# Optimization experiments

Measured on AMD Instinct MI355X. Metric: run time of the kernel, lower is better.

## Reference

```python
import jax, jax.numpy as jnp
import numpy as np

B, C, H, W = 4, 64, 160, 160
OUT = 64
KS = (5, 7)


def conv2d(x, w, b=None, pad=0, groups=1):
    y = jax.lax.conv_general_dilated(
        x, w, (1, 1), [(pad, pad), (pad, pad)],
        feature_group_count=groups,
        dimension_numbers=('NCHW', 'OIHW', 'NCHW'))
    return y if b is None else y + b[None, :, None, None]


def bn_eval(x, g, b, m, v, eps=1e-5):
    s = g / jnp.sqrt(v + eps)
    return x * s[None, :, None, None] + (b - m * s)[None, :, None, None]


def boundary_attn(x, w1, b1, w2, b2):
    Cc = x.shape[1]
    kx = jnp.array([[-1., 0., 1.], [-2., 0., 2.], [-1., 0., 1.]], jnp.float32)
    ky = jnp.array([[-1., -2., -1.], [0., 0., 0.], [1., 2., 1.]], jnp.float32)
    sobel = jnp.concatenate([jnp.tile(kx[None, None], (Cc, 1, 1, 1)),
                             jnp.tile(ky[None, None], (Cc, 1, 1, 1))], axis=0)  # [2C,1,3,3]
    # grouped conv (groups=C): same output-channel grouping semantics as torch
    edge = jnp.abs(conv2d(x, sobel, pad=1, groups=Cc))
    edge = (edge[:, :Cc] + edge[:, Cc:]).mean(axis=1, keepdims=True)
    a = jax.nn.relu(conv2d(x, w1, b1, pad=1))
    a = conv2d(a, w2, b2, pad=0)
    a = jax.nn.sigmoid(a + edge)
    return x * a + x


def icc(off, half_k):
    # iterative cumulative constraint over the (small, static) K channel axis
    K = off.shape[1]
    cs = [None] * K
    cs[half_k] = off[:, half_k]
    for i in range(1, half_k + 1):
        cs[half_k - i] = 0.5 * cs[half_k - i + 1] + 0.5 * off[:, half_k - i]
        cs[half_k + i] = 0.5 * cs[half_k + i - 1] + 0.5 * off[:, half_k + i]
    c = jnp.stack(cs, axis=1)
    w = jnp.ones((K, 1, 3, 3), jnp.float32) / 9.0
    return conv2d(c, w, pad=1, groups=K)


def tumor_center(x):
    _, _, Hx, Wx = x.shape
    fs = x.mean(axis=1)  # [B,H,W]
    hg = jnp.arange(Hx, dtype=x.dtype)[None, :, None]
    wg = jnp.arange(Wx, dtype=x.dtype)[None, None, :]
    tot = fs.sum(axis=(1, 2)) + 1e-6
    return (fs * hg).sum(axis=(1, 2)) / tot, (fs * wg).sum(axis=(1, 2)) / tot


def dyn1d(x, kw, kb, K, O):
    # Original Dynamic1DConv reshapes x to [B*H*W, C, 1, 1] and grid_samples a
    # [1,K] grid per pixel. With align_corners=True a 1x1 input maps every grid
    # coordinate to ix=iy=0, so sampled[n,c,k] == x[b,c,h,w] for all k; the
    # bmm with per-pixel kernels followed by sum over C therefore collapses to
    # (sum_c x) * (sum_k kernels) -- same math, no giant gather materialized.
    Bx, _, Hx, Wx = x.shape
    ker = conv2d(x, kw, kb, pad=0).reshape(Bx, O, K, Hx, Wx)
    return x.sum(axis=1, keepdims=True) * ker.sum(axis=2)


def reference(x, ba_w1, ba_b1, ba_w2, ba_b2,
              off_w1, off_b1, off_bn_g, off_bn_b, off_bn_m, off_bn_v,
              off_w2, off_b2,
              rk5_w, rk5_b, rk7_w, rk7_b,
              lk5_w, lk5_b, lk7_w, lk7_b,
              sf_w, sf_b, sf_bn_g, sf_bn_b, sf_bn_m, sf_bn_v,
              fc_w, fc_b):
    residual = x  # in_channels == out_channels -> nn.Identity
    xa = boundary_attn(x, ba_w1, ba_b1, ba_w2, ba_b2)
    # offset branch (faithful to original; mathematically dead because the
    # per-pixel grid_sample ignores its grid -- see dyn1d). BN in eval mode.
    raw = conv2d(xa, off_w1, off_b1, pad=1)
    raw = jax.nn.relu(bn_eval(raw, off_bn_g, off_bn_b, off_bn_m, off_bn_v))
    raw = conv2d(raw, off_w2, off_b2, pad=1)
    sumk, idx = sum(KS), 0
    _offs = []
    for k in KS:
        _offs.append(icc(jnp.tanh(raw[:, idx:idx + k]), k // 2))
        _offs.append(icc(jnp.tanh(raw[:, sumk + idx:sumk + idx + k]), k // 2))
        idx += k
    _hc, _wc = tumor_center(xa)  # also dead w.r.t. output
    O = OUT // 2 // len(KS)  # 16 channels per scale per flow type
    feats = [dyn1d(xa, rk5_w, rk5_b, 5, O), dyn1d(xa, rk7_w, rk7_b, 7, O),
             dyn1d(xa, lk5_w, lk5_b, 5, O), dyn1d(xa, lk7_w, lk7_b, 7, O)]
    fusion = jnp.concatenate(feats, axis=1)  # [B, OUT, H, W]
    y = jax.nn.relu(bn_eval(conv2d(fusion, sf_w, sf_b, pad=1),
                            sf_bn_g, sf_bn_b, sf_bn_m, sf_bn_v))
    y = conv2d(y, fc_w, fc_b, pad=0)
    return y + residual


def setup_inputs() -> dict:
    key = jax.random.key(0)
    keys = iter(jax.random.split(key, 40))
    def nrm(shape, s=0.05):
        return jax.random.normal(next(keys), shape, jnp.float32) * s
    d = {}
    d['x'] = nrm((B, C, H, W), 1.0)
    d['ba_w1'] = nrm((C // 2, C, 3, 3)); d['ba_b1'] = nrm((C // 2,))
    d['ba_w2'] = nrm((1, C // 2, 1, 1)); d['ba_b2'] = nrm((1,))
    d['off_w1'] = nrm((C // 2, C, 3, 3)); d['off_b1'] = nrm((C // 2,))
    d['off_bn_g'] = 1.0 + nrm((C // 2,)); d['off_bn_b'] = nrm((C // 2,))
    d['off_bn_m'] = nrm((C // 2,))
    d['off_bn_v'] = jax.random.uniform(next(keys), (C // 2,), jnp.float32, 0.5, 1.5)
    d['off_w2'] = nrm((2 * sum(KS), C // 2, 3, 3)); d['off_b2'] = nrm((2 * sum(KS),))
    O = OUT // 2 // len(KS)
    for name, k in (('rk5', 5), ('rk7', 7), ('lk5', 5), ('lk7', 7)):
        d[name + '_w'] = nrm((O * k, C, 1, 1)); d[name + '_b'] = nrm((O * k,))
    d['sf_w'] = nrm((OUT, OUT, 3, 3)); d['sf_b'] = nrm((OUT,))
    d['sf_bn_g'] = 1.0 + nrm((OUT,)); d['sf_bn_b'] = nrm((OUT,))
    d['sf_bn_m'] = nrm((OUT,))
    d['sf_bn_v'] = jax.random.uniform(next(keys), (OUT,), jnp.float32, 0.5, 1.5)
    d['fc_w'] = nrm((OUT, OUT, 1, 1)); d['fc_b'] = nrm((OUT,))
    return d
```

## Files before the change

kernel.cpp:

```cpp
#include <hip/hip_runtime.h>
#include <hip/hip_bf16.h>
#include <math.h>

#define BB 4
#define CC 64
#define HH 160
#define WW 160
#define HWs (HH*WW)
#define NPIX (BB*HWs)

using bf16 = __hip_bfloat16;
typedef __attribute__((ext_vector_type(8))) short short8v;
typedef __attribute__((ext_vector_type(4))) float float4v;

__device__ __forceinline__ unsigned short f2bfu(float f){
    union { bf16 h; unsigned short u; } cv; cv.h = __float2bfloat16(f); return cv.u;
}
__device__ __forceinline__ float bfu2f(unsigned short u){
    union { float f; unsigned int i; } cv; cv.i = ((unsigned int)u)<<16; return cv.f;
}

constexpr int B1X1 = 0;
constexpr int SFBo = 64;
constexpr int SFWf = 128;
constexpr int BAWf = 18560;
constexpr int FUWf = 27776;
constexpr int FCWf = 29824;
constexpr int WS_FLOATS = 31872;

__global__ void k_prep(const float* __restrict__ rk5w, const float* __restrict__ rk5b,
                       const float* __restrict__ rk7w, const float* __restrict__ rk7b,
                       const float* __restrict__ lk5w, const float* __restrict__ lk5b,
                       const float* __restrict__ lk7w, const float* __restrict__ lk7b,
                       const float* __restrict__ sfw,  const float* __restrict__ sfb,
                       const float* __restrict__ bng,  const float* __restrict__ bnb,
                       const float* __restrict__ bnm,  const float* __restrict__ bnv,
                       const float* __restrict__ baw1, const float* __restrict__ fcw,
                       float* __restrict__ ws)
{
    int tid = blockIdx.x*blockDim.x + threadIdx.x;
    int nt  = gridDim.x*blockDim.x;
    for(int o=tid;o<64;o+=nt){
        int grp=o>>4, oo=o&15; int K=(grp&1)?7:5;
        const float* bp = (grp==0)?rk5b:(grp==1)?rk7b:(grp==2)?lk5b:lk7b;
        float s=0.f; for(int k=0;k<K;k++) s += bp[oo*K+k];
        ws[B1X1+o]=s;
    }
    for(int oc=tid;oc<64;oc+=nt){
        float sc = bng[oc]*rsqrtf(bnv[oc]+1e-5f);
        ws[SFBo+oc] = sfb[oc]*sc + bnb[oc] - bnm[oc]*sc;
    }
    unsigned short* sfwf = (unsigned short*)(ws + SFWf);
    for(int idx=tid; idx<36864; idx+=nt){
        int og = idx/9216;  int rem = idx - og*9216;
        int tp = rem/1024;  int rem2 = rem - tp*1024;
        int kc = rem2>>9;   int rem3 = rem2 & 511;
        int lane = rem3>>3; int j = rem3&7;
        int oc = og*16 + (lane&15);
        int ic = kc*32 + (lane>>4)*8 + j;
        float sc = bng[oc]*rsqrtf(bnv[oc]+1e-5f);
        sfwf[idx] = f2bfu(sfw[(oc*64+ic)*9 + tp] * sc);
    }
    unsigned short* bawf = (unsigned short*)(ws + BAWf);
    for(int idx=tid; idx<18432; idx+=nt){
        int og = idx/9216;  int r1 = idx - og*9216;
        int f  = r1/512;    int r2 = r1 & 511;
        int lane = r2>>3;   int j = r2&7;
        int tap = f>>1, kc = f&1;
        int oc = og*16 + (lane&15);
        int ic = kc*32 + (lane>>4)*8 + j;
        bawf[idx] = f2bfu(baw1[(oc*64+ic)*9 + tap]);
    }
    unsigned short* fuwf = (unsigned short*)(ws + FUWf);
    for(int idx=tid; idx<4096; idx+=nt){
        int wave = idx>>10;
        int kc   = (idx>>9)&1;
        int lane = (idx>>3)&63;
        int j    = idx&7;
        int oc = wave*16 + (lane&15);
        int c  = kc*32 + (lane>>4)*8 + j;
        int oo = oc&15; int K = (wave&1)?7:5;
        const float* w = (wave==0)?rk5w:(wave==1)?rk7w:(wave==2)?lk5w:lk7w;
        float s = 0.f;
        for(int k=0;k<K;k++) s += w[(oo*K+k)*64 + c];
        fuwf[idx] = f2bfu(s);
    }
    unsigned short* fcwf = (unsigned short*)(ws + FCWf);
    for(int idx=tid; idx<4096; idx+=nt){
        int wave = idx>>10;
        int kc   = (idx>>9)&1;
        int lane = (idx>>3)&63;
        int j    = idx&7;
        int oc = wave*16 + (lane&15);
        int c  = kc*32 + (lane>>4)*8 + j;
        fcwf[idx] = f2bfu(fcw[oc*64 + c]);
    }
}

__global__ __launch_bounds__(256)
void k_x2nhwc(const float* __restrict__ x, unsigned short* __restrict__ xb)
{
    __shared__ unsigned short ls[128*72];
    const int t = threadIdx.x;
    const int p0 = blockIdx.x*128;
    const int b = p0 / HWs, pp0 = p0 % HWs;
    const float* xbase = x + (size_t)b*CC*HWs + pp0;
    #pragma unroll
    for(int iter=0; iter<32; iter++){
        int idx = iter*256 + t;
        int c = idx>>7, px = idx&127;
        int bs = (c>>3) ^ ((px>>3)&7);
        ls[px*72 + bs*8 + (c&7)] = f2bfu(xbase[(size_t)c*HWs + px]);
    }
    __syncthreads();
    #pragma unroll
    for(int iter=0; iter<4; iter++){
        int idx = iter*256 + t;
        int sub = idx&7, px = idx>>3;
        int bs = sub ^ ((px>>3)&7);
        short8v v = *(short8v*)(ls + px*72 + bs*8);
        *(short8v*)(xb + ((size_t)(p0+px))*64 + sub*8) = v;
    }
}

__global__ __launch_bounds__(256)
void k_fuseA(const unsigned short* __restrict__ xb, const float* __restrict__ bab1,
             const float* __restrict__ baw2, const float* __restrict__ bab2,
             const float* __restrict__ ws, unsigned short* __restrict__ fus)
{
    __shared__ unsigned short tile[10*18*72];
    __shared__ float zbuf[2][8][16];
    __shared__ float ebuf[2][128];
    __shared__ float sxbuf[8][16];
    __shared__ float pbuf[128], qbuf[128];
    const int bw = blockIdx.x, bh = blockIdx.y, b = blockIdx.z;
    const int t = threadIdx.x;
    const int wave = t>>6, lane = t&63;
    const int quad = lane>>4, n = lane&15;
    const int og = wave&1, rh = wave>>1;
    const int w0 = bw*16, h0 = bh*8;

    const unsigned short* fb = xb + (size_t)b*HWs*64;
    for(int idx=t; idx<1440; idx+=256){
        int sub = idx&7; int pix = idx>>3;
        int row = pix/18, col = pix%18;
        int gh = h0-1+row, gw = w0-1+col;
        short8v v = {0,0,0,0,0,0,0,0};
        if(gh>=0&&gh<HH&&gw>=0&&gw<WW)
            v = *(const short8v*)(fb + ((size_t)(gh*WW+gw))*64 + sub*8);
        *(short8v*)(tile + (row*18+col)*72 + sub*8) = v;
    }
    const unsigned short* bawf = (const unsigned short*)(ws + BAWf);
    short8v afrag[18];
    #pragma unroll
    for(int f=0; f<18; f++)
        afrag[f] = *(const short8v*)(bawf + (((size_t)og*18 + f)*64 + lane)*8);
    const unsigned short* fuwf = (const unsigned short*)(ws + FUWf);
    short8v wfrag[2];
    #pragma unroll
    for(int kc=0; kc<2; kc++)
        wfrag[kc] = *(const short8v*)(fuwf + (((size_t)wave*2 + kc)*64 + lane)*8);
    short8v ones;
    #pragma unroll
    for(int j=0;j<8;j++) ones[j] = (short)0x3F80;
    float b1[4], w2[4], bq[4];
    #pragma unroll
    for(int r=0;r<4;r++){
        b1[r] = bab1[og*16 + quad*4 + r];
        w2[r] = baw2[og*16 + quad*4 + r];
        bq[r] = ws[B1X1 + wave*16 + quad*4 + r];
    }
    __syncthreads();

    #pragma unroll
    for(int srp=0; srp<2; srp++){
        const int gr0 = rh*4 + srp*2, gr1 = gr0+1;
        float4v acc0={0,0,0,0}, acc1={0,0,0,0};
        #pragma unroll
        for(int tap=0; tap<9; tap++){
            const int dh = tap/3, dw = tap%3;
            const unsigned short* base0 = tile + ((gr0+dh)*18 + dw + n)*72 + quad*8;
            const unsigned short* base1 = tile + ((gr1+dh)*18 + dw + n)*72 + quad*8;
            #pragma unroll
            for(int kc=0; kc<2; kc++){
                short8v v0 = *(const short8v*)(base0 + kc*32);
                short8v v1 = *(const short8v*)(base1 + kc*32);
                acc0 = __builtin_amdgcn_mfma_f32_16x16x32_bf16(afrag[tap*2+kc], v0, acc0, 0,0,0);
                acc1 = __builtin_amdgcn_mfma_f32_16x16x32_bf16(afrag[tap*2+kc], v1, acc1, 0,0,0);
            }
        }
        float c0 = 0.f, c1 = 0.f;
        #pragma unroll
        for(int r=0;r<4;r++){
            c0 += fmaxf(acc0[r] + b1[r], 0.f) * w2[r];
            c1 += fmaxf(acc1[r] + b1[r], 0.f) * w2[r];
        }
        c0 += __shfl_xor(c0, 16); c0 += __shfl_xor(c0, 32);
        c1 += __shfl_xor(c1, 16); c1 += __shfl_xor(c1, 32);
        if(lane < 16){
            zbuf[og][gr0][lane] = c0;
            zbuf[og][gr1][lane] = c1;
        }
    }

    {
        const int r0 = wave*2, r1 = wave*2+1;
        float4v sa0={0,0,0,0}, sa1={0,0,0,0};
        #pragma unroll
        for(int kc=0; kc<2; kc++){
            short8v v0 = *(const short8v*)(tile + ((r0+1)*18 + 1 + n)*72 + quad*8 + kc*32);
            short8v v1 = *(const short8v*)(tile + ((r1+1)*18 + 1 + n)*72 + quad*8 + kc*32);
            sa0 = __builtin_amdgcn_mfma_f32_16x16x32_bf16(ones, v0, sa0, 0,0,0);
            sa1 = __builtin_amdgcn_mfma_f32_16x16x32_bf16(ones, v1, sa1, 0,0,0);
        }
        if(lane < 16){
            sxbuf[r0][lane] = sa0[0];
            sxbuf[r1][lane] = sa1[0];
        }
    }

    {
        const int half = t>>7, px = t&127;
        const int r = px>>4, c = px&15;
        float e = 0.f;
        #pragma unroll
        for(int s=0; s<4; s++){
            const int sub = half*4 + s;
            if(half==0){
                short8v a0 = *(const short8v*)(tile + ((r  )*18 + c  )*72 + sub*8);
                short8v a2 = *(const short8v*)(tile + ((r  )*18 + c+2)*72 + sub*8);
                short8v a3 = *(const short8v*)(tile + ((r+1)*18 + c  )*72 + sub*8);
                short8v a5 = *(const short8v*)(tile + ((r+1)*18 + c+2)*72 + sub*8);
                short8v a6 = *(const short8v*)(tile + ((r+2)*18 + c  )*72 + sub*8);
                short8v a8 = *(const short8v*)(tile + ((r+2)*18 + c+2)*72 + sub*8);
                #pragma unroll
                for(int j=0;j<8;j++){
                    float gx = (bfu2f((unsigned short)a2[j]) - bfu2f((unsigned short)a0[j]))
                       + 2.f*(bfu2f((unsigned short)a5[j]) - bfu2f((unsigned short)a3[j]))
                       +      (bfu2f((unsigned short)a8[j]) - bfu2f((unsigned short)a6[j]));
                    e += fabsf(gx);
                }
            } else {
                short8v b0 = *(const short8v*)(tile + ((r  )*18 + c  )*72 + sub*8);
                short8v b1v= *(const short8v*)(tile + ((r  )*18 + c+1)*72 + sub*8);
                short8v b2 = *(const short8v*)(tile + ((r  )*18 + c+2)*72 + sub*8);
                short8v b6 = *(const short8v*)(tile + ((r+2)*18 + c  )*72 + sub*8);
                short8v b7 = *(const short8v*)(tile + ((r+2)*18 + c+1)*72 + sub*8);
                short8v b8 = *(const short8v*)(tile + ((r+2)*18 + c+2)*72 + sub*8);
                #pragma unroll
                for(int j=0;j<8;j++){
                    float gy = (bfu2f((unsigned short)b6[j]) - bfu2f((unsigned short)b0[j]))
                       + 2.f*(bfu2f((unsigned short)b7[j]) - bfu2f((unsigned short)b1v[j]))
                       +      (bfu2f((unsigned short)b8[j]) - bfu2f((unsigned short)b2[j]));
                    e += fabsf(gy);
                }
            }
        }
        ebuf[half][px] = e;
    }
    __syncthreads();

    if(t < 128){
        const int row = t>>4, col = t&15;
        float z = zbuf[0][row][col] + zbuf[1][row][col] + bab2[0]
                + (ebuf[0][t] + ebuf[1][t]) * (1.f/32.f);
        float A = 1.f + 1.f/(1.f+__expf(-z));
        float S = A * sxbuf[row][col];
        pbuf[t] = A*S;
        qbuf[t] = S;
    }
    __syncthreads();

    #pragma unroll
    for(int srp=0; srp<4; srp++){
        const int r0 = srp*2, r1 = srp*2+1;
        float4v acc0={0,0,0,0}, acc1={0,0,0,0};
        #pragma unroll
        for(int kc=0; kc<2; kc++){
            short8v v0 = *(const short8v*)(tile + ((r0+1)*18 + 1 + n)*72 + quad*8 + kc*32);
            short8v v1 = *(const short8v*)(tile + ((r1+1)*18 + 1 + n)*72 + quad*8 + kc*32);
            acc0 = __builtin_amdgcn_mfma_f32_16x16x32_bf16(wfrag[kc], v0, acc0, 0,0,0);
            acc1 = __builtin_amdgcn_mfma_f32_16x16x32_bf16(wfrag[kc], v1, acc1, 0,0,0);
        }
        union { unsigned long long u; unsigned short s[4]; } pk0, pk1;
        const int px0 = r0*16 + n, px1 = r1*16 + n;
        const float P0 = pbuf[px0], Q0 = qbuf[px0];
        const float P1 = pbuf[px1], Q1 = qbuf[px1];
        #pragma unroll
        for(int r=0;r<4;r++){
            pk0.s[r] = f2bfu(P0*acc0[r] + Q0*bq[r]);
            pk1.s[r] = f2bfu(P1*acc1[r] + Q1*bq[r]);
        }
        unsigned short* fp0 = fus + ((size_t)b*HWs + (h0+r0)*WW + w0 + n)*64 + wave*16 + quad*4;
        unsigned short* fp1 = fus + ((size_t)b*HWs + (h0+r1)*WW + w0 + n)*64 + wave*16 + quad*4;
        *(unsigned long long*)fp0 = pk0.u;
        *(unsigned long long*)fp1 = pk1.u;
    }
}

__global__ __launch_bounds__(256)
void k_fuseB(const unsigned short* __restrict__ fus, const float* __restrict__ ws,
             const float* __restrict__ fcb, const float* __restrict__ x,
             float* __restrict__ out)
{
    __shared__ unsigned short ftile[10*18*72];
    __shared__ unsigned short ytile[128*72];
    const int bw = blockIdx.x, bh = blockIdx.y, b = blockIdx.z;
    const int t  = threadIdx.x;
    const int wave = t>>6, lane = t&63;
    const int quad = lane>>4, n = lane&15;
    const int w0 = bw*16, h0 = bh*8;

    const unsigned short* fb = fus + (size_t)b*HWs*64;
    for(int idx=t; idx<1440; idx+=256){
        int sub = idx&7; int pix = idx>>3;
        int row = pix/18, col = pix%18;
        int gh = h0-1+row, gw = w0-1+col;
        short8v v = {0,0,0,0,0,0,0,0};
        if(gh>=0&&gh<HH&&gw>=0&&gw<WW)
            v = *(const short8v*)(fb + ((size_t)(gh*WW+gw))*64 + sub*8);
        *(short8v*)(ftile + (row*18+col)*72 + sub*8) = v;
    }
    const unsigned short* sfwf = (const unsigned short*)(ws + SFWf);
    short8v afrag[18];
    #pragma unroll
    for(int f=0; f<18; f++)
        afrag[f] = *(const short8v*)(sfwf + (((size_t)wave*18 + f)*64 + lane)*8);
    const unsigned short* fcwf = (const unsigned short*)(ws + FCWf);
    short8v ffrag[2];
    #pragma unroll
    for(int kc=0; kc<2; kc++)
        ffrag[kc] = *(const short8v*)(fcwf + (((size_t)wave*2 + kc)*64 + lane)*8);
    float bias[4], fb4[4];
    #pragma unroll
    for(int r=0;r<4;r++){
        bias[r] = ws[SFBo + wave*16 + quad*4 + r];
        fb4[r]  = fcb[wave*16 + quad*4 + r];
    }
    __syncthreads();

    #pragma unroll
    for(int srp=0; srp<4; srp++){
        const int r0 = srp*2, r1 = srp*2+1;
        float4v acc0={0,0,0,0}, acc1={0,0,0,0};
        #pragma unroll
        for(int tap=0; tap<9; tap++){
            const int dh = tap/3, dw = tap%3;
            const unsigned short* base0 = ftile + ((r0+dh)*18 + dw + n)*72 + quad*8;
            const unsigned short* base1 = ftile + ((r1+dh)*18 + dw + n)*72 + quad*8;
            #pragma unroll
            for(int kc=0; kc<2; kc++){
                short8v b0 = *(const short8v*)(base0 + kc*32);
                short8v b1 = *(const short8v*)(base1 + kc*32);
                acc0 = __builtin_amdgcn_mfma_f32_16x16x32_bf16(afrag[tap*2+kc], b0, acc0, 0,0,0);
                acc1 = __builtin_amdgcn_mfma_f32_16x16x32_bf16(afrag[tap*2+kc], b1, acc1, 0,0,0);
            }
        }
        union { unsigned long long u; unsigned short s[4]; } pk0, pk1;
        #pragma unroll
        for(int r=0;r<4;r++){
            pk0.s[r] = f2bfu(fmaxf(acc0[r] + bias[r], 0.f));
            pk1.s[r] = f2bfu(fmaxf(acc1[r] + bias[r], 0.f));
        }
        *(unsigned long long*)(ytile + (r0*16+n)*72 + wave*16 + quad*4) = pk0.u;
        *(unsigned long long*)(ytile + (r1*16+n)*72 + wave*16 + quad*4) = pk1.u;
    }
    __syncthreads();

    #pragma unroll
    for(int srp=0; srp<4; srp++){
        const int r0 = srp*2, r1 = srp*2+1;
        float4v acc0={0,0,0,0}, acc1={0,0,0,0};
        #pragma unroll
        for(int kc=0; kc<2; kc++){
            short8v b0 = *(const short8v*)(ytile + (r0*16+n)*72 + quad*8 + kc*32);
            short8v b1 = *(const short8v*)(ytile + (r1*16+n)*72 + quad*8 + kc*32);
            acc0 = __builtin_amdgcn_mfma_f32_16x16x32_bf16(ffrag[kc], b0, acc0, 0,0,0);
            acc1 = __builtin_amdgcn_mfma_f32_16x16x32_bf16(ffrag[kc], b1, acc1, 0,0,0);
        }
        #pragma unroll
        for(int r=0;r<4;r++){
            int oc = wave*16 + quad*4 + r;
            size_t g0 = ((size_t)(b*CC + oc))*HWs + (h0+r0)*WW + w0 + n;
            size_t g1 = ((size_t)(b*CC + oc))*HWs + (h0+r1)*WW + w0 + n;
            out[g0] = acc0[r] + fb4[r] + x[g0];
            out[g1] = acc1[r] + fb4[r] + x[g1];
        }
    }
}

extern "C" void kernel_launch(void* const* d_in, const int* in_sizes, int n_in,
                              void* d_out, int out_size, void* d_ws, size_t ws_size,
                              hipStream_t stream)
{
    const float* x     = (const float*)d_in[0];
    const float* ba_w1 = (const float*)d_in[1];
    const float* ba_b1 = (const float*)d_in[2];
    const float* ba_w2 = (const float*)d_in[3];
    const float* ba_b2 = (const float*)d_in[4];
    const float* rk5_w = (const float*)d_in[13];
    const float* rk5_b = (const float*)d_in[14];
    const float* rk7_w = (const float*)d_in[15];
    const float* rk7_b = (const float*)d_in[16];
    const float* lk5_w = (const float*)d_in[17];
    const float* lk5_b = (const float*)d_in[18];
    const float* lk7_w = (const float*)d_in[19];
    const float* lk7_b = (const float*)d_in[20];
    const float* sf_w  = (const float*)d_in[21];
    const float* sf_b  = (const float*)d_in[22];
    const float* bng   = (const float*)d_in[23];
    const float* bnb   = (const float*)d_in[24];
    const float* bnm   = (const float*)d_in[25];
    const float* bnv   = (const float*)d_in[26];
    const float* fc_w  = (const float*)d_in[27];
    const float* fc_b  = (const float*)d_in[28];

    float* wsf = (float*)d_ws;
    unsigned short* XB  = (unsigned short*)((char*)d_ws + (size_t)WS_FLOATS*4);
    unsigned short* FUS = XB + (size_t)NPIX*64;
    float* out = (float*)d_out;

    k_prep<<<64, 256, 0, stream>>>(rk5_w,rk5_b,rk7_w,rk7_b,lk5_w,lk5_b,lk7_w,lk7_b,
                                   sf_w,sf_b,bng,bnb,bnm,bnv, ba_w1, fc_w, wsf);
    k_x2nhwc<<<NPIX/128, 256, 0, stream>>>(x, XB);
    k_fuseA<<<dim3(10,20,4), 256, 0, stream>>>(XB, ba_b1, ba_w2, ba_b2, wsf, FUS);
    k_fuseB<<<dim3(10,20,4), 256, 0, stream>>>(FUS, wsf, fc_b, x, out);
}
```

Baseline: 182.2 us.

## Switch fused conv kernels from 16x16x32 to 32x32x16 bf16 MFMA tiles

Reorganizes the weight-fragment layouts and the MFMA loops in the boundary-attention, fusion and spatial-fuse kernels to use 32x32x16 bf16 MFMA instructions in place of 16x16x32. Each wave now covers 32 output channels by 32 pixels (two rows of sixteen), and the two-output-group zbuf reduction collapses to one. The aim is to cut the number of MFMA issues and LDS B-fragment reads per output. In exchange it needs larger float16 accumulators, repacks weights per k-chunk, and loads the A fragments per k-chunk inside the loop instead of once up front.

```diff
diff --git a/kernel.cpp b/kernel.cpp
--- a/kernel.cpp
+++ b/kernel.cpp
@@ -10,14 +10,20 @@
 #define NPIX (BB*HWs)
 
 using bf16 = __hip_bfloat16;
-typedef __attribute__((ext_vector_type(8))) short short8v;
-typedef __attribute__((ext_vector_type(4))) float float4v;
+typedef __attribute__((ext_vector_type(8)))  short short8v;
+typedef __attribute__((ext_vector_type(16))) float float16v;
 
 __device__ __forceinline__ unsigned short f2bfu(float f){
     union { bf16 h; unsigned short u; } cv; cv.h = __float2bfloat16(f); return cv.u;
 }
 __device__ __forceinline__ float bfu2f(unsigned short u){
     union { float f; unsigned int i; } cv; cv.i = ((unsigned int)u)<<16; return cv.f;
+}
+__device__ __forceinline__ float16v fzero16(){
+    float16v z;
+    #pragma unroll
+    for(int i=0;i<16;i++) z[i]=0.f;
+    return z;
 }
 
 constexpr int B1X1 = 0;
@@ -52,47 +58,46 @@
     }
     unsigned short* sfwf = (unsigned short*)(ws + SFWf);
     for(int idx=tid; idx<36864; idx+=nt){
-        int og = idx/9216;  int rem = idx - og*9216;
-        int tp = rem/1024;  int rem2 = rem - tp*1024;
-        int kc = rem2>>9;   int rem3 = rem2 & 511;
-        int lane = rem3>>3; int j = rem3&7;
-        int oc = og*16 + (lane&15);
-        int ic = kc*32 + (lane>>4)*8 + j;
+        int og = idx/18432;  int rem = idx - og*18432;
+        int f  = rem>>9;     int r2 = rem & 511;
+        int lane = r2>>3;    int j = r2&7;
+        int tap = f>>2, kc = f&3;
+        int oc = og*32 + (lane&31);
+        int ic = kc*16 + (lane>>5)*8 + j;
         float sc = bng[oc]*rsqrtf(bnv[oc]+1e-5f);
-        sfwf[idx] = f2bfu(sfw[(oc*64+ic)*9 + tp] * sc);
+        sfwf[idx] = f2bfu(sfw[(oc*64+ic)*9 + tap] * sc);
     }
     unsigned short* bawf = (unsigned short*)(ws + BAWf);
     for(int idx=tid; idx<18432; idx+=nt){
-        int og = idx/9216;  int r1 = idx - og*9216;
-        int f  = r1/512;    int r2 = r1 & 511;
-        int lane = r2>>3;   int j = r2&7;
-        int tap = f>>1, kc = f&1;
-        int oc = og*16 + (lane&15);
-        int ic = kc*32 + (lane>>4)*8 + j;
+        int f  = idx>>9;     int r2 = idx & 511;
+        int lane = r2>>3;    int j = r2&7;
+        int tap = f>>2, kc = f&3;
+        int oc = lane&31;
+        int ic = kc*16 + (lane>>5)*8 + j;
         bawf[idx] = f2bfu(baw1[(oc*64+ic)*9 + tap]);
     }
     unsigned short* fuwf = (unsigned short*)(ws + FUWf);
     for(int idx=tid; idx<4096; idx+=nt){
-        int wave = idx>>10;
-        int kc   = (idx>>9)&1;
+        int og   = idx>>11;
+        int kc   = (idx>>9)&3;
         int lane = (idx>>3)&63;
         int j    = idx&7;
-        int oc = wave*16 + (lane&15);
-        int c  = kc*32 + (lane>>4)*8 + j;
-        int oo = oc&15; int K = (wave&1)?7:5;
-        const float* w = (wave==0)?rk5w:(wave==1)?rk7w:(wave==2)?lk5w:lk7w;
+        int oc = og*32 + (lane&31);
+        int c  = kc*16 + (lane>>5)*8 + j;
+        int grp = oc>>4, oo = oc&15; int K = (grp&1)?7:5;
+        const float* w = (grp==0)?rk5w:(grp==1)?rk7w:(grp==2)?lk5w:lk7w;
         float s = 0.f;
         for(int k=0;k<K;k++) s += w[(oo*K+k)*64 + c];
         fuwf[idx] = f2bfu(s);
     }
     unsigned short* fcwf = (unsigned short*)(ws + FCWf);
     for(int idx=tid; idx<4096; idx+=nt){
-        int wave = idx>>10;
-        int kc   = (idx>>9)&1;
+        int og   = idx>>11;
+        int kc   = (idx>>9)&3;
         int lane = (idx>>3)&63;
         int j    = idx&7;
-        int oc = wave*16 + (lane&15);
-        int c  = kc*32 + (lane>>4)*8 + j;
+        int oc = og*32 + (lane&31);
+        int c  = kc*16 + (lane>>5)*8 + j;
         fcwf[idx] = f2bfu(fcw[oc*64 + c]);
     }
 }
@@ -129,15 +134,14 @@
              const float* __restrict__ ws, unsigned short* __restrict__ fus)
 {
     __shared__ unsigned short tile[10*18*72];
-    __shared__ float zbuf[2][8][16];
+    __shared__ float zbuf[8][16];
     __shared__ float ebuf[2][128];
     __shared__ float sxbuf[8][16];
     __shared__ float pbuf[128], qbuf[128];
     const int bw = blockIdx.x, bh = blockIdx.y, b = blockIdx.z;
     const int t = threadIdx.x;
     const int wave = t>>6, lane = t&63;
-    const int quad = lane>>4, n = lane&15;
-    const int og = wave&1, rh = wave>>1;
+    const int half = lane>>5, n = lane&31;
     const int w0 = bw*16, h0 = bh*8;
 
     const unsigned short* fb = xb + (size_t)b*HWs*64;
@@ -150,83 +154,61 @@
             v = *(const short8v*)(fb + ((size_t)(gh*WW+gw))*64 + sub*8);
         *(short8v*)(tile + (row*18+col)*72 + sub*8) = v;
     }
+    float b1v[16], w2v[16];
+    #pragma unroll
+    for(int r=0;r<16;r++){
+        int oc = (r&3) + 8*(r>>2) + 4*half;
+        b1v[r] = bab1[oc];
+        w2v[r] = baw2[oc];
+    }
+    __syncthreads();
+
     const unsigned short* bawf = (const unsigned short*)(ws + BAWf);
-    short8v afrag[18];
-    #pragma unroll
-    for(int f=0; f<18; f++)
-        afrag[f] = *(const short8v*)(bawf + (((size_t)og*18 + f)*64 + lane)*8);
-    const unsigned short* fuwf = (const unsigned short*)(ws + FUWf);
-    short8v wfrag[2];
-    #pragma unroll
-    for(int kc=0; kc<2; kc++)
-        wfrag[kc] = *(const short8v*)(fuwf + (((size_t)wave*2 + kc)*64 + lane)*8);
-    short8v ones;
-    #pragma unroll
-    for(int j=0;j<8;j++) ones[j] = (short)0x3F80;
-    float b1[4], w2[4], bq[4];
-    #pragma unroll
-    for(int r=0;r<4;r++){
-        b1[r] = bab1[og*16 + quad*4 + r];
-        w2[r] = baw2[og*16 + quad*4 + r];
-        bq[r] = ws[B1X1 + wave*16 + quad*4 + r];
-    }
-    __syncthreads();
-
-    #pragma unroll
-    for(int srp=0; srp<2; srp++){
-        const int gr0 = rh*4 + srp*2, gr1 = gr0+1;
-        float4v acc0={0,0,0,0}, acc1={0,0,0,0};
-        #pragma unroll
-        for(int tap=0; tap<9; tap++){
-            const int dh = tap/3, dw = tap%3;
-            const unsigned short* base0 = tile + ((gr0+dh)*18 + dw + n)*72 + quad*8;
-            const unsigned short* base1 = tile + ((gr1+dh)*18 + dw + n)*72 + quad*8;
-            #pragma unroll
-            for(int kc=0; kc<2; kc++){
-                short8v v0 = *(const short8v*)(base0 + kc*32);
-                short8v v1 = *(const short8v*)(base1 + kc*32);
-                acc0 = __builtin_amdgcn_mfma_f32_16x16x32_bf16(afrag[tap*2+kc], v0, acc0, 0,0,0);
-                acc1 = __builtin_amdgcn_mfma_f32_16x16x32_bf16(afrag[tap*2+kc], v1, acc1, 0,0,0);
-            }
-        }
-        float c0 = 0.f, c1 = 0.f;
-        #pragma unroll
-        for(int r=0;r<4;r++){
-            c0 += fmaxf(acc0[r] + b1[r], 0.f) * w2[r];
-            c1 += fmaxf(acc1[r] + b1[r], 0.f) * w2[r];
-        }
-        c0 += __shfl_xor(c0, 16); c0 += __shfl_xor(c0, 32);
-        c1 += __shfl_xor(c1, 16); c1 += __shfl_xor(c1, 32);
-        if(lane < 16){
-            zbuf[og][gr0][lane] = c0;
-            zbuf[og][gr1][lane] = c1;
-        }
-    }
-
-    {
-        const int r0 = wave*2, r1 = wave*2+1;
-        float4v sa0={0,0,0,0}, sa1={0,0,0,0};
-        #pragma unroll
-        for(int kc=0; kc<2; kc++){
-            short8v v0 = *(const short8v*)(tile + ((r0+1)*18 + 1 + n)*72 + quad*8 + kc*32);
-            short8v v1 = *(const short8v*)(tile + ((r1+1)*18 + 1 + n)*72 + quad*8 + kc*32);
-            sa0 = __builtin_amdgcn_mfma_f32_16x16x32_bf16(ones, v0, sa0, 0,0,0);
-            sa1 = __builtin_amdgcn_mfma_f32_16x16x32_bf16(ones, v1, sa1, 0,0,0);
-        }
-        if(lane < 16){
-            sxbuf[r0][lane] = sa0[0];
-            sxbuf[r1][lane] = sa1[0];
-        }
-    }
-
-    {
-        const int half = t>>7, px = t&127;
+    {
+        const int rbase = 2*wave + (n>>4);
+        const int cbase = n&15;
+        float16v acc = fzero16();
+        #pragma unroll
+        for(int kc=0; kc<4; kc++){
+            short8v af[9];
+            #pragma unroll
+            for(int tap=0; tap<9; tap++)
+                af[tap] = *(const short8v*)(bawf + (((size_t)(tap*4+kc))*64 + lane)*8);
+            #pragma unroll
+            for(int tap=0; tap<9; tap++){
+                const int dh = tap/3, dw = tap%3;
+                short8v bf = *(const short8v*)(tile + ((rbase+dh)*18 + cbase+dw)*72
+                                               + kc*16 + half*8);
+                acc = __builtin_amdgcn_mfma_f32_32x32x16_bf16(af[tap], bf, acc, 0,0,0);
+            }
+        }
+        float cz = 0.f;
+        #pragma unroll
+        for(int r=0;r<16;r++) cz += fmaxf(acc[r]+b1v[r],0.f)*w2v[r];
+        cz += __shfl_xor(cz, 32);
+        if(lane < 32) zbuf[2*wave + (n>>4)][n&15] = cz;
+    }
+    {
+        short8v ones;
+        #pragma unroll
+        for(int j=0;j<8;j++) ones[j] = (short)0x3F80;
+        float16v s = fzero16();
+        const int rr = 2*wave + (n>>4) + 1, cc = (n&15) + 1;
+        #pragma unroll
+        for(int kc=0; kc<4; kc++){
+            short8v bf = *(const short8v*)(tile + (rr*18 + cc)*72 + kc*16 + half*8);
+            s = __builtin_amdgcn_mfma_f32_32x32x16_bf16(ones, bf, s, 0,0,0);
+        }
+        if(lane < 32) sxbuf[2*wave + (n>>4)][n&15] = s[0];
+    }
+    {
+        const int hf = t>>7, px = t&127;
         const int r = px>>4, c = px&15;
         float e = 0.f;
         #pragma unroll
         for(int s=0; s<4; s++){
-            const int sub = half*4 + s;
-            if(half==0){
+            const int sub = hf*4 + s;
+            if(hf==0){
                 short8v a0 = *(const short8v*)(tile + ((r  )*18 + c  )*72 + sub*8);
                 short8v a2 = *(const short8v*)(tile + ((r  )*18 + c+2)*72 + sub*8);
                 short8v a3 = *(const short8v*)(tile + ((r+1)*18 + c  )*72 + sub*8);
@@ -242,7 +224,7 @@
                 }
             } else {
                 short8v b0 = *(const short8v*)(tile + ((r  )*18 + c  )*72 + sub*8);
-                short8v b1v= *(const short8v*)(tile + ((r  )*18 + c+1)*72 + sub*8);
+                short8v b1 = *(const short8v*)(tile + ((r  )*18 + c+1)*72 + sub*8);
                 short8v b2 = *(const short8v*)(tile + ((r  )*18 + c+2)*72 + sub*8);
                 short8v b6 = *(const short8v*)(tile + ((r+2)*18 + c  )*72 + sub*8);
                 short8v b7 = *(const short8v*)(tile + ((r+2)*18 + c+1)*72 + sub*8);
@@ -250,19 +232,19 @@
                 #pragma unroll
                 for(int j=0;j<8;j++){
                     float gy = (bfu2f((unsigned short)b6[j]) - bfu2f((unsigned short)b0[j]))
-                       + 2.f*(bfu2f((unsigned short)b7[j]) - bfu2f((unsigned short)b1v[j]))
+                       + 2.f*(bfu2f((unsigned short)b7[j]) - bfu2f((unsigned short)b1[j]))
                        +      (bfu2f((unsigned short)b8[j]) - bfu2f((unsigned short)b2[j]));
                     e += fabsf(gy);
                 }
             }
         }
-        ebuf[half][px] = e;
+        ebuf[hf][px] = e;
     }
     __syncthreads();
 
     if(t < 128){
         const int row = t>>4, col = t&15;
-        float z = zbuf[0][row][col] + zbuf[1][row][col] + bab2[0]
+        float z = zbuf[row][col] + bab2[0]
                 + (ebuf[0][t] + ebuf[1][t]) * (1.f/32.f);
         float A = 1.f + 1.f/(1.f+__expf(-z));
         float S = A * sxbuf[row][col];
@@ -271,30 +253,39 @@
     }
     __syncthreads();
 
-    #pragma unroll
-    for(int srp=0; srp<4; srp++){
-        const int r0 = srp*2, r1 = srp*2+1;
-        float4v acc0={0,0,0,0}, acc1={0,0,0,0};
-        #pragma unroll
-        for(int kc=0; kc<2; kc++){
-            short8v v0 = *(const short8v*)(tile + ((r0+1)*18 + 1 + n)*72 + quad*8 + kc*32);
-            short8v v1 = *(const short8v*)(tile + ((r1+1)*18 + 1 + n)*72 + quad*8 + kc*32);
-            acc0 = __builtin_amdgcn_mfma_f32_16x16x32_bf16(wfrag[kc], v0, acc0, 0,0,0);
-            acc1 = __builtin_amdgcn_mfma_f32_16x16x32_bf16(wfrag[kc], v1, acc1, 0,0,0);
-        }
-        union { unsigned long long u; unsigned short s[4]; } pk0, pk1;
-        const int px0 = r0*16 + n, px1 = r1*16 + n;
-        const float P0 = pbuf[px0], Q0 = qbuf[px0];
-        const float P1 = pbuf[px1], Q1 = qbuf[px1];
-        #pragma unroll
-        for(int r=0;r<4;r++){
-            pk0.s[r] = f2bfu(P0*acc0[r] + Q0*bq[r]);
-            pk1.s[r] = f2bfu(P1*acc1[r] + Q1*bq[r]);
-        }
-        unsigned short* fp0 = fus + ((size_t)b*HWs + (h0+r0)*WW + w0 + n)*64 + wave*16 + quad*4;
-        unsigned short* fp1 = fus + ((size_t)b*HWs + (h0+r1)*WW + w0 + n)*64 + wave*16 + quad*4;
-        *(unsigned long long*)fp0 = pk0.u;
-        *(unsigned long long*)fp1 = pk1.u;
+    {
+        const int og = wave&1;
+        const unsigned short* fuwf = (const unsigned short*)(ws + FUWf);
+        short8v wf[4];
+        #pragma unroll
+        for(int kc=0; kc<4; kc++)
+            wf[kc] = *(const short8v*)(fuwf + (((size_t)og*4 + kc)*64 + lane)*8);
+        float bqv[16];
+        #pragma unroll
+        for(int r=0;r<16;r++) bqv[r] = ws[B1X1 + og*32 + (r&3)+8*(r>>2)+4*half];
+        #pragma unroll
+        for(int t2=0; t2<2; t2++){
+            const int rp = (wave>>1) + 2*t2;
+            const int row = 2*rp + (n>>4), col = n&15;
+            float16v a = fzero16();
+            #pragma unroll
+            for(int kc=0; kc<4; kc++){
+                short8v bf = *(const short8v*)(tile + ((row+1)*18 + col+1)*72
+                                               + kc*16 + half*8);
+                a = __builtin_amdgcn_mfma_f32_32x32x16_bf16(wf[kc], bf, a, 0,0,0);
+            }
+            const float P = pbuf[row*16+col], Q = qbuf[row*16+col];
+            unsigned short* base = fus + ((size_t)b*HWs + (h0+row)*WW + w0+col)*64
+                                   + og*32 + 4*half;
+            #pragma unroll
+            for(int g=0; g<4; g++){
+                union { unsigned long long u; unsigned short s[4]; } pk;
+                #pragma unroll
+                for(int rr=0; rr<4; rr++)
+                    pk.s[rr] = f2bfu(P*a[4*g+rr] + Q*bqv[4*g+rr]);
+                *(unsigned long long*)(base + 8*g) = pk.u;
+            }
+        }
     }
 }
 
@@ -308,7 +299,8 @@
     const int bw = blockIdx.x, bh = blockIdx.y, b = blockIdx.z;
     const int t  = threadIdx.x;
     const int wave = t>>6, lane = t&63;
-    const int quad = lane>>4, n = lane&15;
+    const int half = lane>>5, n = lane&31;
+    const int og = wave&1;
     const int w0 = bw*16, h0 = bh*8;
 
     const unsigned short* fb = fus + (size_t)b*HWs*64;
@@ -321,70 +313,75 @@
             v = *(const short8v*)(fb + ((size_t)(gh*WW+gw))*64 + sub*8);
         *(short8v*)(ftile + (row*18+col)*72 + sub*8) = v;
     }
+    float biasv[16];
+    #pragma unroll
+    for(int r=0;r<16;r++) biasv[r] = ws[SFBo + og*32 + (r&3)+8*(r>>2)+4*half];
+    __syncthreads();
+
     const unsigned short* sfwf = (const unsigned short*)(ws + SFWf);
-    short8v afrag[18];
-    #pragma unroll
-    for(int f=0; f<18; f++)
-        afrag[f] = *(const short8v*)(sfwf + (((size_t)wave*18 + f)*64 + lane)*8);
-    const unsigned short* fcwf = (const unsigned short*)(ws + FCWf);
-    short8v ffrag[2];
-    #pragma unroll
-    for(int kc=0; kc<2; kc++)
-        ffrag[kc] = *(const short8v*)(fcwf + (((size_t)wave*2 + kc)*64 + lane)*8);
-    float bias[4], fb4[4];
-    #pragma unroll
-    for(int r=0;r<4;r++){
-        bias[r] = ws[SFBo + wave*16 + quad*4 + r];
-        fb4[r]  = fcb[wave*16 + quad*4 + r];
-    }
-    __syncthreads();
-
-    #pragma unroll
-    for(int srp=0; srp<4; srp++){
-        const int r0 = srp*2, r1 = srp*2+1;
-        float4v acc0={0,0,0,0}, acc1={0,0,0,0};
-        #pragma unroll
-        for(int tap=0; tap<9; tap++){
-            const int dh = tap/3, dw = tap%3;
-            const unsigned short* base0 = ftile + ((r0+dh)*18 + dw + n)*72 + quad*8;
-            const unsigned short* base1 = ftile + ((r1+dh)*18 + dw + n)*72 + quad*8;
-            #pragma unroll
-            for(int kc=0; kc<2; kc++){
-                short8v b0 = *(const short8v*)(base0 + kc*32);
-                short8v b1 = *(const short8v*)(base1 + kc*32);
-                acc0 = __builtin_amdgcn_mfma_f32_16x16x32_bf16(afrag[tap*2+kc], b0, acc0, 0,0,0);
-                acc1 = __builtin_amdgcn_mfma_f32_16x16x32_bf16(afrag[tap*2+kc], b1, acc1, 0,0,0);
-            }
-        }
-        union { unsigned long long u; unsigned short s[4]; } pk0, pk1;
-        #pragma unroll
-        for(int r=0;r<4;r++){
-            pk0.s[r] = f2bfu(fmaxf(acc0[r] + bias[r], 0.f));
-            pk1.s[r] = f2bfu(fmaxf(acc1[r] + bias[r], 0.f));
-        }
-        *(unsigned long long*)(ytile + (r0*16+n)*72 + wave*16 + quad*4) = pk0.u;
-        *(unsigned long long*)(ytile + (r1*16+n)*72 + wave*16 + quad*4) = pk1.u;
-    }
-    __syncthreads();
-
-    #pragma unroll
-    for(int srp=0; srp<4; srp++){
-        const int r0 = srp*2, r1 = srp*2+1;
-        float4v acc0={0,0,0,0}, acc1={0,0,0,0};
-        #pragma unroll
-        for(int kc=0; kc<2; kc++){
-            short8v b0 = *(const short8v*)(ytile + (r0*16+n)*72 + quad*8 + kc*32);
-            short8v b1 = *(const short8v*)(ytile + (r1*16+n)*72 + quad*8 + kc*32);
-            acc0 = __builtin_amdgcn_mfma_f32_16x16x32_bf16(ffrag[kc], b0, acc0, 0,0,0);
-            acc1 = __builtin_amdgcn_mfma_f32_16x16x32_bf16(ffrag[kc], b1, acc1, 0,0,0);
-        }
-        #pragma unroll
-        for(int r=0;r<4;r++){
-            int oc = wave*16 + quad*4 + r;
-            size_t g0 = ((size_t)(b*CC + oc))*HWs + (h0+r0)*WW + w0 + n;
-            size_t g1 = ((size_t)(b*CC + oc))*HWs + (h0+r1)*WW + w0 + n;
-            out[g0] = acc0[r] + fb4[r] + x[g0];
-            out[g1] = acc1[r] + fb4[r] + x[g1];
+    const int rp0 = wave>>1, rp1 = rp0+2;
+    const int row0 = 2*rp0 + (n>>4), row1 = 2*rp1 + (n>>4), col = n&15;
+    {
+        float16v A0 = fzero16(), A1 = fzero16();
+        #pragma unroll
+        for(int kc=0; kc<4; kc++){
+            short8v af[9];
+            #pragma unroll
+            for(int tap=0; tap<9; tap++)
+                af[tap] = *(const short8v*)(sfwf + (((size_t)og*36 + tap*4+kc)*64 + lane)*8);
+            #pragma unroll
+            for(int tap=0; tap<9; tap++){
+                const int dh = tap/3, dw = tap%3;
+                short8v b0 = *(const short8v*)(ftile + ((row0+dh)*18 + col+dw)*72
+                                               + kc*16 + half*8);
+                short8v b1 = *(const short8v*)(ftile + ((row1+dh)*18 + col+dw)*72
+                                               + kc*16 + half*8);
+                A0 = __builtin_amdgcn_mfma_f32_32x32x16_bf16(af[tap], b0, A0, 0,0,0);
+                A1 = __builtin_amdgcn_mfma_f32_32x32x16_bf16(af[tap], b1, A1, 0,0,0);
+            }
+        }
+        unsigned short* y0 = ytile + (row0*16+col)*72 + og*32 + 4*half;
+        unsigned short* y1p = ytile + (row1*16+col)*72 + og*32 + 4*half;
+        #pragma unroll
+        for(int g=0; g<4; g++){
+            union { unsigned long long u; unsigned short s[4]; } pk0, pk1;
+            #pragma unroll
+            for(int rr=0; rr<4; rr++){
+                pk0.s[rr] = f2bfu(fmaxf(A0[4*g+rr] + biasv[4*g+rr], 0.f));
+                pk1.s[rr] = f2bfu(fmaxf(A1[4*g+rr] + biasv[4*g+rr], 0.f));
+            }
+            *(unsigned long long*)(y0  + 8*g) = pk0.u;
+            *(unsigned long long*)(y1p + 8*g) = pk1.u;
+        }
+    }
+    __syncthreads();
+
+    {
+        const unsigned short* fcwf = (const unsigned short*)(ws + FCWf);
+        short8v ff[4];
+        #pragma unroll
+        for(int kc=0; kc<4; kc++)
+            ff[kc] = *(const short8v*)(fcwf + (((size_t)og*4 + kc)*64 + lane)*8);
+        float fcbv[16];
+        #pragma unroll
+        for(int r=0;r<16;r++) fcbv[r] = fcb[og*32 + (r&3)+8*(r>>2)+4*half];
+        #pragma unroll
+        for(int t2=0; t2<2; t2++){
+            const int rp = (wave>>1) + 2*t2;
+            const int row = 2*rp + (n>>4);
+            const int px = row*16 + col;
+            float16v F = fzero16();
+            #pragma unroll
+            for(int kc=0; kc<4; kc++){
+                short8v bf = *(const short8v*)(ytile + px*72 + kc*16 + half*8);
+                F = __builtin_amdgcn_mfma_f32_32x32x16_bf16(ff[kc], bf, F, 0,0,0);
+            }
+            #pragma unroll
+            for(int r=0;r<16;r++){
+                int oc = og*32 + (r&3)+8*(r>>2)+4*half;
+                size_t g = ((size_t)(b*CC + oc))*HWs + (h0+row)*WW + w0 + col;
+                out[g] = F[r] + fcbv[r] + x[g];
+            }
         }
     }
 }
```

Result: no change. 184.9 us (+1.5%).
